# Performance work log

Measured on AMD Instinct MI355X. Metric: run time of the kernel, lower is better.

## Reference

```python
import jax, jax.numpy as jnp
import numpy as np
import math

B, T, D, H = 8, 1024, 512, 8
DH = D // H          # attention dim per head = 64
VS = D               # values_size


def pos_emb(t2, d):
    """TENER relative positional encoding, shape [t2, d], positions -t2/2 .. t2/2-1."""
    half = d // 2
    pos = jnp.arange(-t2 // 2, t2 // 2, dtype=jnp.float32)[:, None]            # [t2,1]
    div = jnp.exp(jnp.arange(half, dtype=jnp.float32) * -(math.log(10000.0) / (half - 1)))
    ang = pos * div[None, :]                                                    # [t2,half]
    return jnp.concatenate([jnp.sin(ang), jnp.cos(ang)], axis=1)               # [t2,d]


def shift(t):
    """Skew trick: [b,n,T,2T] relative logits -> [b,n,T,T] aligned logits."""
    b, n, ts, _ = t.shape
    zp = jnp.zeros((b, n, ts, 1), t.dtype)
    t = jnp.concatenate([t, zp], axis=-1).reshape(b, n, 2 * ts + 1, ts)
    t = t[:, :, :-1].reshape(b, n, ts, 2 * ts)
    return t[:, :, :, ts:]


def setup_inputs() -> dict:
    key = jax.random.key(0)
    ks = jax.random.split(key, 7)
    s = 1.0 / math.sqrt(D)
    return {
        "query": jax.random.normal(ks[0], (B, T, D), jnp.float32),
        "key_in": jax.random.normal(ks[1], (B, T, D), jnp.float32),
        "value": jax.random.normal(ks[2], (B, T, D), jnp.float32),
        "mask": jnp.ones((B, T), jnp.int32),
        "Wq": jax.random.normal(ks[3], (D, D), jnp.float32) * s,
        "bq": jnp.zeros((D,), jnp.float32),
        "Wv": jax.random.normal(ks[4], (D, VS), jnp.float32) * s,
        "bv": jnp.zeros((VS,), jnp.float32),
        "Wo": jax.random.normal(ks[5], (VS, D), jnp.float32) * s,
        "bo": jnp.zeros((D,), jnp.float32),
        "v_bias": jax.random.normal(ks[6], (H, DH), jnp.float32) * 0.1,
    }


def reference(query, key_in, value, mask, Wq, bq, Wv, bv, Wo, bo, v_bias):
    pe = pos_emb(2 * T, DH)                                                     # [2T, DH]
    # NOTE: key is NOT projected in the original module; only a reshape.
    k = key_in.reshape(B, T, H, DH).transpose(0, 2, 1, 3)                       # [B,H,T,DH]
    q = (query @ Wq + bq).reshape(B, T, H, DH).transpose(0, 2, 1, 3)            # [B,H,T,DH]
    v = (value @ Wv + bv).reshape(B, T, H, VS // H).transpose(0, 2, 1, 3)       # [B,H,T,VS/H]
    qk = jnp.einsum('bnqd,bnkd->bnqk', q, k)                                    # content logits
    qr = jnp.einsum('bnqd,ld->bnql', q, pe)                                     # [B,H,T,2T]
    vb = jnp.einsum('nd,ld->nl', v_bias, pe)[None, :, None, :]                  # [1,H,1,2T]
    rel = shift(qr + vb)                                                        # [B,H,T,T]
    attn = qk + rel                                                             # no 1/sqrt(d) scaling (TENER)
    attn = jnp.where(mask[:, None, None, :] == 0, -jnp.inf, attn)
    attn = jax.nn.softmax(attn, axis=-1)
    x = jnp.einsum('bnij,bnjv->binv', attn, v).reshape(B, T, VS)
    return x @ Wo + bo
```

## Files before the change

### kernel.cpp

```cpp
#include <hip/hip_runtime.h>
#include <hip/hip_bf16.h>

typedef __bf16 bf16;
typedef __bf16 bf16x8 __attribute__((ext_vector_type(8)));
typedef __bf16 bf16x4 __attribute__((ext_vector_type(4)));
typedef float f32x4 __attribute__((ext_vector_type(4)));

#define NEGBIG (-3.0e38f)

__device__ inline f32x4 mfma16(bf16x8 a, bf16x8 b, f32x4 c) {
    return __builtin_amdgcn_mfma_f32_16x16x32_bf16(a, b, c, 0, 0, 0);
}
__device__ inline bf16x8 ld8(const bf16* p) { return *reinterpret_cast<const bf16x8*>(p); }
__device__ inline f32x4 ldf4(const float* p) { return *reinterpret_cast<const f32x4*>(p); }

template<int CTRL>
__device__ inline float rowror(float x) {
    int xi = __builtin_bit_cast(int, x);
    int yi = __builtin_amdgcn_update_dpp(xi, xi, CTRL, 0xF, 0xF, false);
    return __builtin_bit_cast(float, yi);
}
__device__ inline float rowmax16(float x) {
    x = fmaxf(x, rowror<0x121>(x));
    x = fmaxf(x, rowror<0x122>(x));
    x = fmaxf(x, rowror<0x124>(x));
    x = fmaxf(x, rowror<0x128>(x));
    return x;
}
__device__ inline float rowsum16(float x) {
    x += rowror<0x121>(x);
    x += rowror<0x122>(x);
    x += rowror<0x124>(x);
    x += rowror<0x128>(x);
    return x;
}

__global__ __launch_bounds__(256) void tables_kernel(const float* __restrict__ W0, const float* __restrict__ W1,
                                                     const float* __restrict__ W2, bf16* __restrict__ pe2,
                                                     bf16* __restrict__ T0, bf16* __restrict__ T1,
                                                     bf16* __restrict__ T2) {
    __shared__ float tile[64][65];
    int bid = blockIdx.x;
    if (bid < 256) {
        int g = bid * 256 + threadIdx.x;
        int j = g >> 6, d = g & 63;
        float w = __expf(-(float)(d & 31) * 0.29710775393471563f);
        float ang = (float)j * w;
        float v = (d < 32) ? sinf(ang) : cosf(ang);
        int idx = (((j >> 4) << 1) + (d >> 5)) * 512 + (((d >> 3) & 3) * 16 + (j & 15)) * 8 + (d & 7);
        pe2[idx] = (bf16)v;
    } else {
        int wb = bid - 256;
        int which = wb >> 6, bidx = wb & 63;
        const float* W = which == 0 ? W0 : which == 1 ? W1 : W2;
        bf16* Wt = which == 0 ? T0 : which == 1 ? T1 : T2;
        int tx = bidx & 7, ty = bidx >> 3;
        int lane = threadIdx.x & 63, w = threadIdx.x >> 6;
        #pragma unroll
        for (int i = 0; i < 16; i++) {
            int k = ty * 64 + w * 16 + i;
            tile[w * 16 + i][lane] = W[k * 512 + tx * 64 + lane];
        }
        __syncthreads();
        #pragma unroll
        for (int i = 0; i < 16; i++) {
            int n = tx * 64 + w * 16 + i;
            Wt[n * 512 + ty * 64 + lane] = (bf16)tile[lane][w * 16 + i];
        }
    }
}

__global__ void kcvt_kernel(const float* __restrict__ kin, bf16* __restrict__ kw) {
    int i = (blockIdx.x * 256 + threadIdx.x) * 4;
    f32x4 v = ldf4(kin + i);
    int dh = i & 63, hh = (i >> 6) & 7, t = (i >> 9) & 1023, b = i >> 19;
    int bh = (b << 3) + hh;
    bf16x4 o;
    #pragma unroll
    for (int e = 0; e < 4; e++) o[e] = (bf16)v[e];
    int blk = ((bh << 6) + (t >> 4)) * 2 + (dh >> 5);
    int off = (((dh >> 3) & 3) * 16 + (t & 15)) * 8 + (dh & 7);
    *reinterpret_cast<bf16x4*>(kw + blk * 512 + off) = o;
}

__global__ void qaug_kernel(const bf16* __restrict__ qw, const float* __restrict__ v_bias,
                            bf16* __restrict__ q2) {
    int g = blockIdx.x * 256 + threadIdx.x;
    int row = g >> 5, dp = g & 31;
    int t = row & 1023, h = (row >> 10) & 7;
    float qs = (float)qw[row * 64 + dp];
    float qc = (float)qw[row * 64 + 32 + dp];
    float as = qs + v_bias[h * 64 + dp];
    float ac = qc + v_bias[h * 64 + 32 + dp];
    float w = __expf(-(float)dp * 0.29710775393471563f);
    float sa, ca;
    __sincosf((float)t * w, &sa, &ca);
    q2[row * 64 + dp]      = (bf16)(as * ca + ac * sa);
    q2[row * 64 + 32 + dp] = (bf16)(ac * ca - as * sa);
}

__global__ __launch_bounds__(256) void proj_qv(const float* __restrict__ Q, const float* __restrict__ V,
                                               const bf16* __restrict__ WtQ, const bf16* __restrict__ WtV,
                                               const float* __restrict__ bq, const float* __restrict__ bv,
                                               bf16* __restrict__ q_ws, bf16* __restrict__ v_ws) {
    __shared__ bf16 As[64][40];
    __shared__ bf16 Bs[64][40];
    int isv = blockIdx.z;
    const float* A = isv ? V : Q;
    const bf16* Wt = isv ? WtV : WtQ;
    const float* bias = isv ? bv : bq;
    int row0 = blockIdx.x * 64, n0 = blockIdx.y * 64;
    int tid = threadIdx.x, lane = tid & 63, w = tid >> 6, lg = lane >> 4, lr = lane & 15;
    int wm = (w >> 1) * 32, wn = (w & 1) * 32;
    f32x4 acc[2][2] = {};
    for (int k0 = 0; k0 < 512; k0 += 32) {
        int r = tid >> 2, kq = (tid & 3) * 8;
        f32x4 a0 = ldf4(A + (row0 + r) * 512 + k0 + kq);
        f32x4 a1 = ldf4(A + (row0 + r) * 512 + k0 + kq + 4);
        bf16x8 av;
        #pragma unroll
        for (int e = 0; e < 4; e++) { av[e] = (bf16)a0[e]; av[4 + e] = (bf16)a1[e]; }
        bf16x8 bv8 = ld8(Wt + (n0 + r) * 512 + k0 + kq);
        __syncthreads();
        *reinterpret_cast<bf16x8*>(&As[r][kq]) = av;
        *reinterpret_cast<bf16x8*>(&Bs[r][kq]) = bv8;
        __syncthreads();
        bf16x8 aa0 = ld8(&As[wm + lr][lg * 8]);
        bf16x8 aa1 = ld8(&As[wm + 16 + lr][lg * 8]);
        bf16x8 bb0 = ld8(&Bs[wn + lr][lg * 8]);
        bf16x8 bb1 = ld8(&Bs[wn + 16 + lr][lg * 8]);
        acc[0][0] = mfma16(aa0, bb0, acc[0][0]);
        acc[0][1] = mfma16(aa0, bb1, acc[0][1]);
        acc[1][0] = mfma16(aa1, bb0, acc[1][0]);
        acc[1][1] = mfma16(aa1, bb1, acc[1][1]);
    }
    #pragma unroll
    for (int mi = 0; mi < 2; mi++)
    #pragma unroll
    for (int ni = 0; ni < 2; ni++) {
        int rowb = row0 + wm + mi * 16 + lg * 4;
        int col = n0 + wn + ni * 16 + lr;
        int b = rowb >> 10, t = rowb & 1023, hh = col >> 6, dh = col & 63;
        int bh = (b << 3) + hh;
        if (isv) {
            int blk = (((bh << 4) + (t >> 6)) * 2 + ((t >> 5) & 1)) * 4 + (dh >> 4);
            int off = (((t >> 3) & 3) * 16 + (dh & 15)) * 8 + (t & 7);
            bf16x4 o4;
            #pragma unroll
            for (int rr = 0; rr < 4; rr++) o4[rr] = (bf16)((float)acc[mi][ni][rr] + bias[col]);
            *reinterpret_cast<bf16x4*>(v_ws + blk * 512 + off) = o4;
        } else {
            #pragma unroll
            for (int rr = 0; rr < 4; rr++) {
                float v = (float)acc[mi][ni][rr] + bias[col];
                q_ws[((bh << 10) + t + rr) * 64 + dh] = (bf16)v;
            }
        }
    }
}

__global__ __launch_bounds__(256) void proj_o(const bf16* __restrict__ Ap, const bf16* __restrict__ Wt,
                                              const float* __restrict__ bias, float* __restrict__ outp) {
    __shared__ bf16 As[64][40];
    __shared__ bf16 Bs[64][40];
    int row0 = blockIdx.x * 64, n0 = blockIdx.y * 64;
    int tid = threadIdx.x, lane = tid & 63, w = tid >> 6, lg = lane >> 4, lr = lane & 15;
    int wm = (w >> 1) * 32, wn = (w & 1) * 32;
    f32x4 acc[2][2] = {};
    for (int k0 = 0; k0 < 512; k0 += 32) {
        int r = tid >> 2, kq = (tid & 3) * 8;
        bf16x8 av = ld8(Ap + (row0 + r) * 512 + k0 + kq);
        bf16x8 bv = ld8(Wt + (n0 + r) * 512 + k0 + kq);
        __syncthreads();
        *reinterpret_cast<bf16x8*>(&As[r][kq]) = av;
        *reinterpret_cast<bf16x8*>(&Bs[r][kq]) = bv;
        __syncthreads();
        bf16x8 a0 = ld8(&As[wm + lr][lg * 8]);
        bf16x8 a1 = ld8(&As[wm + 16 + lr][lg * 8]);
        bf16x8 b0 = ld8(&Bs[wn + lr][lg * 8]);
        bf16x8 b1 = ld8(&Bs[wn + 16 + lr][lg * 8]);
        acc[0][0] = mfma16(a0, b0, acc[0][0]);
        acc[0][1] = mfma16(a0, b1, acc[0][1]);
        acc[1][0] = mfma16(a1, b0, acc[1][0]);
        acc[1][1] = mfma16(a1, b1, acc[1][1]);
    }
    #pragma unroll
    for (int mi = 0; mi < 2; mi++)
    #pragma unroll
    for (int ni = 0; ni < 2; ni++) {
        int rowb = row0 + wm + mi * 16 + lg * 4;
        int col = n0 + wn + ni * 16 + lr;
        #pragma unroll
        for (int rr = 0; rr < 4; rr++)
            outp[(rowb + rr) * 512 + col] = (float)acc[mi][ni][rr] + bias[col];
    }
}

__global__ __launch_bounds__(256, 4) void tener_attn(const bf16* __restrict__ qw, const bf16* __restrict__ q2,
                                                     const bf16* __restrict__ kw, const bf16* __restrict__ vt,
                                                     const int* __restrict__ mask, const bf16* __restrict__ pe2,
                                                     bf16* __restrict__ xw) {
    __shared__ bf16 Pl[4][16][76];
    __shared__ float Mo[4][16], Do[4][16];
    __shared__ float Oo[2][16][65];
    int bh = blockIdx.x, b = bh >> 3, h = bh & 7;
    (void)h;
    int tid = threadIdx.x, w = tid >> 6, lane = tid & 63, lg = lane >> 4, lr = lane & 15;
    int rbase = (blockIdx.y * 2 + (w >> 1)) * 16;
    int jh = w & 1;

    const int* mkb = mask + (b << 10);

    int qoff = ((bh << 10) + rbase + lr) * 64 + lg * 8;
    bf16x8 aq0 = ld8(qw + qoff);
    bf16x8 aq1 = ld8(qw + qoff + 32);
    bf16x8 aq2 = ld8(q2 + qoff);
    bf16x8 aq3 = ld8(q2 + qoff + 32);

    f32x4 o[4] = {};
    float m_[4], d_[4];
    #pragma unroll
    for (int r = 0; r < 4; r++) { m_[r] = NEGBIG; d_[r] = 0.f; }

    for (int tt = 0; tt < 8; tt++) {
        __builtin_amdgcn_sched_barrier(0x7F);

        int j0 = jh * 512 + tt * 64;

        f32x4 s[4];
        int kblk = (bh << 6) + (j0 >> 4);
        int pblk = j0 >> 4;
        #pragma unroll
        for (int nt = 0; nt < 4; nt++) {
            const bf16* kp = kw + (((kblk + nt) << 1)) * 512 + lane * 8;
            const bf16* pp = pe2 + (((pblk + nt) << 1)) * 512 + lane * 8;
            f32x4 acc = {};
            acc = mfma16(aq0, ld8(kp), acc);
            acc = mfma16(aq1, ld8(kp + 512), acc);
            acc = mfma16(aq2, ld8(pp), acc);
            acc = mfma16(aq3, ld8(pp + 512), acc);
            s[nt] = acc;
        }

        int mk[4];
        #pragma unroll
        for (int nt = 0; nt < 4; nt++) mk[nt] = mkb[j0 + nt * 16 + lr];

        #pragma unroll
        for (int r = 0; r < 4; r++) {
            int rl = 4 * lg + r;
            float sv[4];
            #pragma unroll
            for (int nt = 0; nt < 4; nt++) sv[nt] = mk[nt] ? (float)s[nt][r] : NEGBIG;
            float mx = fmaxf(fmaxf(sv[0], sv[1]), fmaxf(sv[2], sv[3]));
            mx = rowmax16(mx);
            float nm = fmaxf(m_[r], mx);
            float sc = __expf(m_[r] - nm);
            float p[4], rs = 0.f;
            #pragma unroll
            for (int nt = 0; nt < 4; nt++) {
                p[nt] = mk[nt] ? __expf(sv[nt] - nm) : 0.f;
                rs += p[nt];
            }
            rs = rowsum16(rs);
            d_[r] = d_[r] * sc + rs;
            m_[r] = nm;
            #pragma unroll
            for (int dt = 0; dt < 4; dt++) o[dt][r] *= sc;
            #pragma unroll
            for (int nt = 0; nt < 4; nt++) Pl[w][rl][nt * 16 + lr] = (bf16)p[nt];
        }

        __builtin_amdgcn_sched_barrier(0x7F);

        int vblk0 = ((((bh << 4) + (j0 >> 6)) << 1)) << 2;
        #pragma unroll
        for (int ks = 0; ks < 2; ks++) {
            bf16x8 ap = ld8(&Pl[w][lr][ks * 32 + lg * 8]);
            #pragma unroll
            for (int dt = 0; dt < 4; dt++) {
                const bf16* vp = vt + (vblk0 + (ks << 2) + dt) * 512 + lane * 8;
                o[dt] = mfma16(ap, ld8(vp), o[dt]);
            }
        }
    }

    if (w & 1) {
        #pragma unroll
        for (int dt = 0; dt < 4; dt++)
        #pragma unroll
        for (int r = 0; r < 4; r++)
            Oo[w >> 1][4 * lg + r][dt * 16 + lr] = o[dt][r];
        if (lr == 0) {
            #pragma unroll
            for (int r = 0; r < 4; r++) { Mo[w][4 * lg + r] = m_[r]; Do[w][4 * lg + r] = d_[r]; }
        }
    }
    __syncthreads();
    if (!(w & 1)) {
        #pragma unroll
        for (int r = 0; r < 4; r++) {
            int rl = 4 * lg + r;
            float m1 = Mo[w | 1][rl], d1 = Do[w | 1][rl];
            float m = fmaxf(m_[r], m1);
            float a0 = __expf(m_[r] - m), a1 = __expf(m1 - m);
            float dd = d_[r] * a0 + d1 * a1;
            float inv = dd > 0.f ? 1.f / dd : 0.f;
            int row = rbase + rl;
            #pragma unroll
            for (int dt = 0; dt < 4; dt++) {
                float v = (o[dt][r] * a0 + Oo[w >> 1][rl][dt * 16 + lr] * a1) * inv;
                xw[(((b << 10) + row) << 9) + ((bh & 7) << 6) + dt * 16 + lr] = (bf16)v;
            }
        }
    }
}

extern "C" void kernel_launch(void* const* d_in, const int* in_sizes, int n_in,
                              void* d_out, int out_size, void* d_ws, size_t ws_size,
                              hipStream_t stream) {
    const float* query  = (const float*)d_in[0];
    const float* key_in = (const float*)d_in[1];
    const float* value  = (const float*)d_in[2];
    const int*   mask   = (const int*)d_in[3];
    const float* Wq     = (const float*)d_in[4];
    const float* bq     = (const float*)d_in[5];
    const float* Wv     = (const float*)d_in[6];
    const float* bv     = (const float*)d_in[7];
    const float* Wo     = (const float*)d_in[8];
    const float* bo     = (const float*)d_in[9];
    const float* v_bias = (const float*)d_in[10];

    char* ws = (char*)d_ws;
    bf16*  pe2  = (bf16*)(ws);
    bf16*  q_ws = (bf16*)(ws + 327680);
    bf16*  v_ws = (bf16*)(ws + 327680 + 8388608);
    bf16*  x_ws = (bf16*)(ws + 327680 + 16777216);
    bf16*  wt_q = (bf16*)(ws + 327680 + 25165824);
    bf16*  wt_v = (bf16*)(ws + 327680 + 25690112);
    bf16*  wt_o = (bf16*)(ws + 327680 + 26214400);
    bf16*  k_ws = (bf16*)d_out;
    bf16*  q2_ws = (bf16*)((char*)d_out + 8388608);

    tables_kernel<<<448, 256, 0, stream>>>(Wq, Wv, Wo, pe2, wt_q, wt_v, wt_o);
    kcvt_kernel<<<4096, 256, 0, stream>>>(key_in, k_ws);
    proj_qv<<<dim3(128, 8, 2), 256, 0, stream>>>(query, value, wt_q, wt_v, bq, bv, q_ws, v_ws);
    qaug_kernel<<<8192, 256, 0, stream>>>(q_ws, v_bias, q2_ws);
    tener_attn<<<dim3(64, 32), 256, 0, stream>>>(q_ws, q2_ws, k_ws, v_ws, mask, pe2, x_ws);
    proj_o<<<dim3(128, 8), 256, 0, stream>>>(x_ws, wt_o, bo, (float*)d_out);
}
```

Before: 122.0 us.

## Fuse key conversion into tables kernel and q-rotation into attention; lazy softmax rescale

Merges the key fp32-to-bf16 relayout into the tables kernel launch and removes the separate qaug kernel by computing the rotated positional query operands inside the attention kernel from registers. This drops two launches and the q2 round trip through global memory. It also skips the online-softmax rescale of the accumulators whenever the running max does not grow across the wavefront. In exchange, every attention block recomputes sincos per query element, and the skip adds a wave-uniform branch.

```diff
diff --git a/kernel.cpp b/kernel.cpp
--- a/kernel.cpp
+++ b/kernel.cpp
@@ -36,9 +36,10 @@
 }
 
 __global__ __launch_bounds__(256) void tables_kernel(const float* __restrict__ W0, const float* __restrict__ W1,
-                                                     const float* __restrict__ W2, bf16* __restrict__ pe2,
-                                                     bf16* __restrict__ T0, bf16* __restrict__ T1,
-                                                     bf16* __restrict__ T2) {
+                                                     const float* __restrict__ W2, const float* __restrict__ kin,
+                                                     bf16* __restrict__ pe2, bf16* __restrict__ T0,
+                                                     bf16* __restrict__ T1, bf16* __restrict__ T2,
+                                                     bf16* __restrict__ kw) {
     __shared__ float tile[64][65];
     int bid = blockIdx.x;
     if (bid < 256) {
@@ -49,7 +50,7 @@
         float v = (d < 32) ? sinf(ang) : cosf(ang);
         int idx = (((j >> 4) << 1) + (d >> 5)) * 512 + (((d >> 3) & 3) * 16 + (j & 15)) * 8 + (d & 7);
         pe2[idx] = (bf16)v;
-    } else {
+    } else if (bid < 448) {
         int wb = bid - 256;
         int which = wb >> 6, bidx = wb & 63;
         const float* W = which == 0 ? W0 : which == 1 ? W1 : W2;
@@ -67,36 +68,18 @@
             int n = tx * 64 + w * 16 + i;
             Wt[n * 512 + ty * 64 + lane] = (bf16)tile[lane][w * 16 + i];
         }
-    }
-}
-
-__global__ void kcvt_kernel(const float* __restrict__ kin, bf16* __restrict__ kw) {
-    int i = (blockIdx.x * 256 + threadIdx.x) * 4;
-    f32x4 v = ldf4(kin + i);
-    int dh = i & 63, hh = (i >> 6) & 7, t = (i >> 9) & 1023, b = i >> 19;
-    int bh = (b << 3) + hh;
-    bf16x4 o;
-    #pragma unroll
-    for (int e = 0; e < 4; e++) o[e] = (bf16)v[e];
-    int blk = ((bh << 6) + (t >> 4)) * 2 + (dh >> 5);
-    int off = (((dh >> 3) & 3) * 16 + (t & 15)) * 8 + (dh & 7);
-    *reinterpret_cast<bf16x4*>(kw + blk * 512 + off) = o;
-}
-
-__global__ void qaug_kernel(const bf16* __restrict__ qw, const float* __restrict__ v_bias,
-                            bf16* __restrict__ q2) {
-    int g = blockIdx.x * 256 + threadIdx.x;
-    int row = g >> 5, dp = g & 31;
-    int t = row & 1023, h = (row >> 10) & 7;
-    float qs = (float)qw[row * 64 + dp];
-    float qc = (float)qw[row * 64 + 32 + dp];
-    float as = qs + v_bias[h * 64 + dp];
-    float ac = qc + v_bias[h * 64 + 32 + dp];
-    float w = __expf(-(float)dp * 0.29710775393471563f);
-    float sa, ca;
-    __sincosf((float)t * w, &sa, &ca);
-    q2[row * 64 + dp]      = (bf16)(as * ca + ac * sa);
-    q2[row * 64 + 32 + dp] = (bf16)(ac * ca - as * sa);
+    } else {
+        int i = ((bid - 448) * 256 + threadIdx.x) * 4;
+        f32x4 v = ldf4(kin + i);
+        int dh = i & 63, hh = (i >> 6) & 7, t = (i >> 9) & 1023, b = i >> 19;
+        int bh = (b << 3) + hh;
+        bf16x4 o;
+        #pragma unroll
+        for (int e = 0; e < 4; e++) o[e] = (bf16)v[e];
+        int blk = ((bh << 6) + (t >> 4)) * 2 + (dh >> 5);
+        int off = (((dh >> 3) & 3) * 16 + (t & 15)) * 8 + (dh & 7);
+        *reinterpret_cast<bf16x4*>(kw + blk * 512 + off) = o;
+    }
 }
 
 __global__ __launch_bounds__(256) void proj_qv(const float* __restrict__ Q, const float* __restrict__ V,
@@ -196,15 +179,14 @@
     }
 }
 
-__global__ __launch_bounds__(256, 4) void tener_attn(const bf16* __restrict__ qw, const bf16* __restrict__ q2,
-                                                     const bf16* __restrict__ kw, const bf16* __restrict__ vt,
-                                                     const int* __restrict__ mask, const bf16* __restrict__ pe2,
+__global__ __launch_bounds__(256, 4) void tener_attn(const bf16* __restrict__ qw, const bf16* __restrict__ kw,
+                                                     const bf16* __restrict__ vt, const int* __restrict__ mask,
+                                                     const bf16* __restrict__ pe2, const float* __restrict__ v_bias,
                                                      bf16* __restrict__ xw) {
     __shared__ bf16 Pl[4][16][76];
     __shared__ float Mo[4][16], Do[4][16];
     __shared__ float Oo[2][16][65];
     int bh = blockIdx.x, b = bh >> 3, h = bh & 7;
-    (void)h;
     int tid = threadIdx.x, w = tid >> 6, lane = tid & 63, lg = lane >> 4, lr = lane & 15;
     int rbase = (blockIdx.y * 2 + (w >> 1)) * 16;
     int jh = w & 1;
@@ -214,8 +196,23 @@
     int qoff = ((bh << 10) + rbase + lr) * 64 + lg * 8;
     bf16x8 aq0 = ld8(qw + qoff);
     bf16x8 aq1 = ld8(qw + qoff + 32);
-    bf16x8 aq2 = ld8(q2 + qoff);
-    bf16x8 aq3 = ld8(q2 + qoff + 32);
+
+    bf16x8 aq2, aq3;
+    {
+        int t = rbase + lr;
+        const float* vbp = v_bias + (h << 6) + lg * 8;
+        #pragma unroll
+        for (int e = 0; e < 8; e++) {
+            int d = lg * 8 + e;
+            float as = (float)aq0[e] + vbp[e];
+            float ac = (float)aq1[e] + vbp[32 + e];
+            float w_ = __expf(-(float)d * 0.29710775393471563f);
+            float sa, ca;
+            __sincosf((float)t * w_, &sa, &ca);
+            aq2[e] = (bf16)(as * ca + ac * sa);
+            aq3[e] = (bf16)(ac * ca - as * sa);
+        }
+    }
 
     f32x4 o[4] = {};
     float m_[4], d_[4];
@@ -254,19 +251,22 @@
             for (int nt = 0; nt < 4; nt++) sv[nt] = mk[nt] ? (float)s[nt][r] : NEGBIG;
             float mx = fmaxf(fmaxf(sv[0], sv[1]), fmaxf(sv[2], sv[3]));
             mx = rowmax16(mx);
-            float nm = fmaxf(m_[r], mx);
-            float sc = __expf(m_[r] - nm);
+            if (!__all(mx <= m_[r])) {
+                float nm = fmaxf(m_[r], mx);
+                float sc = __expf(m_[r] - nm);
+                d_[r] *= sc;
+                #pragma unroll
+                for (int dt = 0; dt < 4; dt++) o[dt][r] *= sc;
+                m_[r] = nm;
+            }
             float p[4], rs = 0.f;
             #pragma unroll
             for (int nt = 0; nt < 4; nt++) {
-                p[nt] = mk[nt] ? __expf(sv[nt] - nm) : 0.f;
+                p[nt] = mk[nt] ? __expf(sv[nt] - m_[r]) : 0.f;
                 rs += p[nt];
             }
             rs = rowsum16(rs);
-            d_[r] = d_[r] * sc + rs;
-            m_[r] = nm;
-            #pragma unroll
-            for (int dt = 0; dt < 4; dt++) o[dt][r] *= sc;
+            d_[r] += rs;
             #pragma unroll
             for (int nt = 0; nt < 4; nt++) Pl[w][rl][nt * 16 + lr] = (bf16)p[nt];
         }
@@ -310,7 +310,7 @@
             #pragma unroll
             for (int dt = 0; dt < 4; dt++) {
                 float v = (o[dt][r] * a0 + Oo[w >> 1][rl][dt * 16 + lr] * a1) * inv;
-                xw[(((b << 10) + row) << 9) + ((bh & 7) << 6) + dt * 16 + lr] = (bf16)v;
+                xw[(((b << 10) + row) << 9) + (h << 6) + dt * 16 + lr] = (bf16)v;
             }
         }
     }
@@ -340,12 +340,9 @@
     bf16*  wt_v = (bf16*)(ws + 327680 + 25690112);
     bf16*  wt_o = (bf16*)(ws + 327680 + 26214400);
     bf16*  k_ws = (bf16*)d_out;
-    bf16*  q2_ws = (bf16*)((char*)d_out + 8388608);
-
-    tables_kernel<<<448, 256, 0, stream>>>(Wq, Wv, Wo, pe2, wt_q, wt_v, wt_o);
-    kcvt_kernel<<<4096, 256, 0, stream>>>(key_in, k_ws);
+
+    tables_kernel<<<4544, 256, 0, stream>>>(Wq, Wv, Wo, key_in, pe2, wt_q, wt_v, wt_o, k_ws);
     proj_qv<<<dim3(128, 8, 2), 256, 0, stream>>>(query, value, wt_q, wt_v, bq, bv, q_ws, v_ws);
-    qaug_kernel<<<8192, 256, 0, stream>>>(q_ws, v_bias, q2_ws);
-    tener_attn<<<dim3(64, 32), 256, 0, stream>>>(q_ws, q2_ws, k_ws, v_ws, mask, pe2, x_ws);
+    tener_attn<<<dim3(64, 32), 256, 0, stream>>>(q_ws, k_ws, v_ws, mask, pe2, v_bias, x_ws);
     proj_o<<<dim3(128, 8), 256, 0, stream>>>(x_ws, wt_o, bo, (float*)d_out);
 }
```

Measured after the change: 118.6 us. -2.8%, faster.
